# Optimization experiments

Hardware: AMD Instinct MI355X
Metric: run time of the kernel (lower is better)

The kernel has to match this reference:

```python
import jax, jax.numpy as jnp
import numpy as np

B, S, D, H = 4, 1024, 1024, 16
DH = D // H  # 64, per-head dim; FFN hidden = 2048
DFF = 2048

def setup_inputs() -> dict:
    key = jax.random.key(0)
    ks = jax.random.split(key, 6)
    x = jax.random.normal(ks[0], (B, S, D), dtype=jnp.float32)
    # Per-head q/k/v projection weights, stacked over heads: [H, D, DH].
    # Equivalent math to n_heads separate SelfAttentionLayer(d_head) calls + concat.
    sc_in = 1.0 / np.sqrt(D)
    Wq = jax.random.normal(ks[1], (H, D, DH), dtype=jnp.float32) * sc_in
    Wk = jax.random.normal(ks[2], (H, D, DH), dtype=jnp.float32) * sc_in
    Wv = jax.random.normal(ks[3], (H, D, DH), dtype=jnp.float32) * sc_in
    W1 = jax.random.normal(ks[4], (D, DFF), dtype=jnp.float32) * sc_in
    b1 = jnp.zeros((DFF,), dtype=jnp.float32)
    W2 = jax.random.normal(ks[5], (DFF, D), dtype=jnp.float32) * (1.0 / np.sqrt(DFF))
    b2 = jnp.zeros((D,), dtype=jnp.float32)
    return {"x": x, "Wq": Wq, "Wk": Wk, "Wv": Wv,
            "W1": W1, "b1": b1, "W2": W2, "b2": b2}

def reference(x, Wq, Wk, Wv, W1, b1, W2, b2):
    # Batched multi-head self-attention (math-equivalent to the per-head loop + concat).
    q = jnp.einsum('bsd,hde->bhse', x, Wq)          # [B,H,S,DH]
    k = jnp.einsum('bsd,hde->bhse', x, Wk)
    v = jnp.einsum('bsd,hde->bhse', x, Wv)
    scale = 1.0 / jnp.sqrt(jnp.asarray(q.shape[-1], q.dtype))
    scores = jnp.einsum('bhqe,bhke->bhqk', q, k) * scale  # [B,H,S,S]
    attn = jax.nn.softmax(scores, axis=-1)
    o = jnp.einsum('bhqk,bhke->bhqe', attn, v)      # [B,H,S,DH]
    h1 = o.transpose(0, 2, 1, 3).reshape(x.shape[0], x.shape[1], -1)  # concat heads -> [B,S,D]
    # FCLayer(2048, d): Dense(2048, relu) -> Dense(d)
    y = jax.nn.relu(h1 @ W1 + b1) @ W2 + b2
    return y
```

## Files before the change

### kernel.cpp

```cpp
#include <hip/hip_runtime.h>
#include <hip/hip_bf16.h>


typedef unsigned short u16;
typedef __attribute__((ext_vector_type(8))) short bfrag8;
typedef __attribute__((ext_vector_type(4))) float f32x4;
typedef __attribute__((ext_vector_type(4))) int ix4;

constexpr int Bb = 4, Ss = 1024, Dd = 1024, Hh = 16, DFF = 2048;
constexpr float QSCALE = 0.18033688011112042f;

__device__ __forceinline__ u16 f2bf(float f) {
  unsigned u = __float_as_uint(f);
  return (u16)((u + 0x7fffu + ((u >> 16) & 1u)) >> 16);
}

__device__ __forceinline__ void gload16(const void* g, void* l) {
  __builtin_amdgcn_global_load_lds(
      (const __attribute__((address_space(1))) unsigned int*)g,
      (__attribute__((address_space(3))) unsigned int*)l, 16, 0, 0);
}

__device__ __forceinline__ int xcd_swz() {
  const int id = blockIdx.y * gridDim.x + blockIdx.x;
  const int cpx = (gridDim.x * gridDim.y) >> 3;
  return (id & 7) * cpx + (id >> 3);
}

__global__ __launch_bounds__(256) void cvt_bf16(const float* __restrict__ in,
                                                u16* __restrict__ out, int n4) {
  int i = blockIdx.x * 256 + threadIdx.x;
  if (i >= n4) return;
  float4 v = ((const float4*)in)[i];
  ushort4 o = make_ushort4(f2bf(v.x), f2bf(v.y), f2bf(v.z), f2bf(v.w));
  *(ushort4*)(out + (size_t)i * 4) = o;
}

__device__ __forceinline__ void transpose64(const float* __restrict__ in,
                                            u16* __restrict__ out,
                                            int R, int C, int r0, int c0) {
  __shared__ float tile[64][65];
  const int t = threadIdx.x, cl = t & 63, rq = t >> 6;
#pragma unroll
  for (int i = 0; i < 16; ++i) {
    int rl = rq * 16 + i;
    tile[rl][cl] = in[(size_t)(r0 + rl) * C + c0 + cl];
  }
  __syncthreads();
#pragma unroll
  for (int i = 0; i < 16; ++i) {
    int oc = rq * 16 + i;
    out[(size_t)(c0 + oc) * R + r0 + cl] = f2bf(tile[cl][oc]);
  }
}

__global__ __launch_bounds__(256) void transpose_cvt(const float* __restrict__ in,
                                                     u16* __restrict__ out,
                                                     int R, int C) {
  transpose64(in, out, R, C, blockIdx.x * 64, blockIdx.y * 64);
}

__global__ __launch_bounds__(256) void qkv_transpose_cvt(
    const float* __restrict__ Wq, const float* __restrict__ Wk,
    const float* __restrict__ Wv, u16* __restrict__ out) {
  const int z = blockIdx.y;
  const int which = z >> 4, h = z & 15;
  const float* in = (which == 0 ? Wq : which == 1 ? Wk : Wv) + (size_t)h * 1024 * 64;
  u16* o = out + (size_t)z * 64 * 1024;
  transpose64(in, o, 1024, 64, blockIdx.x * 64, 0);
}

template <int EPI>
__global__ __launch_bounds__(256) void mfma_gemm(
    const u16* __restrict__ A, const u16* __restrict__ Bt,
    const float* __restrict__ bias, void* __restrict__ Cout, int N, int K) {
  __shared__ alignas(16) u16 Asm[128 * 32];
  __shared__ alignas(16) u16 Bsm[128 * 32];
  const int tid = threadIdx.x;
  const int wid = tid >> 6, lane = tid & 63;
  const int nid = xcd_swz();
  const int m0 = (nid / gridDim.x) * 128, n0 = (nid % gridDim.x) * 128;
  const int wr = wid >> 1, wc = wid & 1;
  const int fr = lane & 15, krow = lane >> 4;

  const int srow = tid >> 2;
  const int sk = (tid & 3) * 8;
  const u16* ga0 = A + (size_t)(m0 + srow) * K + sk;
  const u16* ga1 = A + (size_t)(m0 + srow + 64) * K + sk;
  const u16* gb0 = Bt + (size_t)(n0 + srow) * K + sk;
  const u16* gb1 = Bt + (size_t)(n0 + srow + 64) * K + sk;
  char* lA0 = (char*)Asm + tid * 16;
  char* lA1 = lA0 + 4096;
  char* lB0 = (char*)Bsm + tid * 16;
  char* lB1 = lB0 + 4096;

  f32x4 acc[4][4];
#pragma unroll
  for (int i = 0; i < 4; ++i)
#pragma unroll
    for (int j = 0; j < 4; ++j) acc[i][j] = (f32x4){0.f, 0.f, 0.f, 0.f};

  const char* pa = (const char*)Asm + (wr * 64 + fr) * 64 + krow * 16;
  const char* pb = (const char*)Bsm + (wc * 64 + fr) * 64 + krow * 16;

  for (int kt = 0; kt < K / 32; ++kt) {
    __syncthreads();
    gload16(ga0 + kt * 32, lA0);
    gload16(ga1 + kt * 32, lA1);
    gload16(gb0 + kt * 32, lB0);
    gload16(gb1 + kt * 32, lB1);
    __syncthreads();

    bfrag8 af[4], bfv[4];
#pragma unroll
    for (int i = 0; i < 4; ++i) af[i] = *(const bfrag8*)(pa + i * 1024);
#pragma unroll
    for (int j = 0; j < 4; ++j) bfv[j] = *(const bfrag8*)(pb + j * 1024);
#pragma unroll
    for (int i = 0; i < 4; ++i)
#pragma unroll
      for (int j = 0; j < 4; ++j)
        acc[i][j] = __builtin_amdgcn_mfma_f32_16x16x32_bf16(af[i], bfv[j], acc[i][j], 0, 0, 0);
  }

  const int orow = (lane >> 4) * 4;
  const int ocol = lane & 15;
#pragma unroll
  for (int i = 0; i < 4; ++i) {
#pragma unroll
    for (int j = 0; j < 4; ++j) {
      const int gn = n0 + wc * 64 + j * 16 + ocol;
      const int gm0 = m0 + wr * 64 + i * 16 + orow;
      if (EPI == 0) {
        const int which = gn >> 10, hh = (gn >> 6) & 15, e = gn & 63;
        const int bb = gm0 >> 10, s0 = gm0 & 1023;
        const int hb = hh * 4 + bb;
        u16* oq = (u16*)Cout;
        if (which == 0) {
#pragma unroll
          for (int r = 0; r < 4; ++r)
            oq[((size_t)hb * 1024 + s0 + r) * 64 + e] = f2bf(acc[i][j][r] * QSCALE);
        } else if (which == 1) {
#pragma unroll
          for (int r = 0; r < 4; ++r)
            oq[4194304 + ((size_t)hb * 1024 + s0 + r) * 64 + e] = f2bf(acc[i][j][r]);
        } else {
          ushort4 pk = make_ushort4(f2bf(acc[i][j][0]), f2bf(acc[i][j][1]),
                                    f2bf(acc[i][j][2]), f2bf(acc[i][j][3]));
          *(ushort4*)&oq[8388608 + ((size_t)hb * 64 + e) * 1024 + s0] = pk;
        }
      } else if (EPI == 1) {
#pragma unroll
        for (int r = 0; r < 4; ++r) {
          float v = fmaxf(acc[i][j][r] + bias[gn], 0.f);
          ((u16*)Cout)[(size_t)(gm0 + r) * N + gn] = f2bf(v);
        }
      } else {
#pragma unroll
        for (int r = 0; r < 4; ++r)
          ((float*)Cout)[(size_t)(gm0 + r) * N + gn] = acc[i][j][r] + bias[gn];
      }
    }
  }
}

__global__ __launch_bounds__(256) void mfma_gemm_n64(
    const u16* __restrict__ A, const u16* __restrict__ Bt,
    const float* __restrict__ bias, float* __restrict__ Cout, int N, int K) {
  __shared__ alignas(16) u16 Asm[128 * 32];
  __shared__ alignas(16) u16 Bsm[64 * 32];
  const int tid = threadIdx.x;
  const int wid = tid >> 6, lane = tid & 63;
  const int nid = xcd_swz();
  const int m0 = (nid / gridDim.x) * 128, n0 = (nid % gridDim.x) * 64;
  const int fr = lane & 15, krow = lane >> 4;

  const int srow = tid >> 2;
  const int sk = (tid & 3) * 8;
  const u16* ga0 = A + (size_t)(m0 + srow) * K + sk;
  const u16* ga1 = A + (size_t)(m0 + srow + 64) * K + sk;
  const u16* gb0 = Bt + (size_t)(n0 + srow) * K + sk;
  char* lA0 = (char*)Asm + tid * 16;
  char* lA1 = lA0 + 4096;
  char* lB0 = (char*)Bsm + tid * 16;

  f32x4 acc[2][4];
#pragma unroll
  for (int i = 0; i < 2; ++i)
#pragma unroll
    for (int j = 0; j < 4; ++j) acc[i][j] = (f32x4){0.f, 0.f, 0.f, 0.f};

  const char* pa = (const char*)Asm + (wid * 32 + fr) * 64 + krow * 16;
  const char* pb = (const char*)Bsm + fr * 64 + krow * 16;

  for (int kt = 0; kt < K / 32; ++kt) {
    __syncthreads();
    gload16(ga0 + kt * 32, lA0);
    gload16(ga1 + kt * 32, lA1);
    gload16(gb0 + kt * 32, lB0);
    __syncthreads();

    bfrag8 af[2], bfv[4];
#pragma unroll
    for (int i = 0; i < 2; ++i) af[i] = *(const bfrag8*)(pa + i * 1024);
#pragma unroll
    for (int j = 0; j < 4; ++j) bfv[j] = *(const bfrag8*)(pb + j * 1024);
#pragma unroll
    for (int i = 0; i < 2; ++i)
#pragma unroll
      for (int j = 0; j < 4; ++j)
        acc[i][j] = __builtin_amdgcn_mfma_f32_16x16x32_bf16(af[i], bfv[j], acc[i][j], 0, 0, 0);
  }

  const int orow = (lane >> 4) * 4;
  const int ocol = lane & 15;
#pragma unroll
  for (int i = 0; i < 2; ++i)
#pragma unroll
    for (int j = 0; j < 4; ++j) {
      const int gn = n0 + j * 16 + ocol;
      const int gm0 = m0 + wid * 32 + i * 16 + orow;
#pragma unroll
      for (int r = 0; r < 4; ++r)
        Cout[(size_t)(gm0 + r) * N + gn] = acc[i][j][r] + bias[gn];
    }
}

__global__ __launch_bounds__(256, 2) void attn_mfma(
    const u16* __restrict__ qb, const u16* __restrict__ kb,
    const u16* __restrict__ vtb, u16* __restrict__ h1) {
  const int tid = threadIdx.x, wid = tid >> 6, lane = tid & 63;
  const int nid = xcd_swz();
  const int qx = nid & 7, hb = nid >> 3;
  const int h = hb >> 2, b = hb & 3;
  const int q0 = qx * 128 + wid * 32;
  const int fr = lane & 15, hi = lane >> 4;

  const u16* Qg = qb + ((size_t)hb * 1024 + q0) * 64;
  const u16* Kg = kb + (size_t)hb * 1024 * 64;
  const u16* Vg = vtb + (size_t)hb * 64 * 1024;

  bfrag8 qf[2][2];
#pragma unroll
  for (int m = 0; m < 2; ++m)
#pragma unroll
    for (int kk = 0; kk < 2; ++kk)
      qf[m][kk] = *(const bfrag8*)(Qg + (m * 16 + fr) * 64 + kk * 32 + hi * 8);

  f32x4 acc2[2][4];
#pragma unroll
  for (int m = 0; m < 2; ++m)
#pragma unroll
    for (int en = 0; en < 4; ++en) acc2[m][en] = (f32x4){0.f, 0.f, 0.f, 0.f};
  float mrun[2] = {-1e30f, -1e30f}, lrun[2] = {0.f, 0.f};

  const int addrA = ((lane & 15) + ((lane & 16) << 1)) << 2;
  const int addrB = addrA + 64;
  const bool hiSel = (lane >= 32);

  bfrag8 kfA[4][2], vfA[4][2], kfB[4][2], vfB[4][2];

#define LOAD_KV(kf, vf, kt)                                                    \
  {                                                                            \
    _Pragma("unroll") for (int kn = 0; kn < 4; ++kn)                           \
        _Pragma("unroll") for (int kk = 0; kk < 2; ++kk) {                     \
      kf[kn][kk] = *(const bfrag8*)(Kg + (size_t)((kt)*64 + kn * 16 + fr) * 64 \
                                    + kk * 32 + hi * 8);                       \
      vf[kn][kk] = *(const bfrag8*)(Vg + (size_t)(kn * 16 + fr) * 1024         \
                                    + (kt)*64 + kk * 32 + hi * 8);             \
    }                                                                          \
  }

#define TILE_STEP(kf, vf)                                                      \
  {                                                                            \
    f32x4 sc2[2][4];                                                           \
    __builtin_amdgcn_s_setprio(1);                                             \
    _Pragma("unroll") for (int m = 0; m < 2; ++m)                              \
        _Pragma("unroll") for (int kn = 0; kn < 4; ++kn) {                     \
      f32x4 t = (f32x4){0.f, 0.f, 0.f, 0.f};                                   \
      t = __builtin_amdgcn_mfma_f32_16x16x32_bf16(kf[kn][0], qf[m][0], t, 0, 0, 0); \
      t = __builtin_amdgcn_mfma_f32_16x16x32_bf16(kf[kn][1], qf[m][1], t, 0, 0, 0); \
      sc2[m][kn] = t;                                                          \
    }                                                                          \
    __builtin_amdgcn_s_setprio(0);                                             \
    int pk[2][4][2];                                                           \
    _Pragma("unroll") for (int m = 0; m < 2; ++m) {                            \
      float cm = -1e30f;                                                       \
      _Pragma("unroll") for (int kn = 0; kn < 4; ++kn)                         \
          _Pragma("unroll") for (int r = 0; r < 4; ++r)                        \
              cm = fmaxf(cm, sc2[m][kn][r]);                                   \
      cm = fmaxf(cm, __shfl_xor(cm, 16));                                      \
      cm = fmaxf(cm, __shfl_xor(cm, 32));                                      \
      const float mnew = fmaxf(mrun[m], cm);                                   \
      const float scl = exp2f(mrun[m] - mnew);                                 \
      mrun[m] = mnew;                                                          \
      float psum = 0.f;                                                        \
      float p[4][4];                                                           \
      _Pragma("unroll") for (int kn = 0; kn < 4; ++kn)                         \
          _Pragma("unroll") for (int r = 0; r < 4; ++r) {                      \
        p[kn][r] = exp2f(sc2[m][kn][r] - mnew);                                \
        psum += p[kn][r];                                                      \
      }                                                                        \
      psum += __shfl_xor(psum, 16);                                            \
      psum += __shfl_xor(psum, 32);                                            \
      lrun[m] = lrun[m] * scl + psum;                                          \
      _Pragma("unroll") for (int en = 0; en < 4; ++en)                         \
          acc2[m][en] = acc2[m][en] * scl;                                     \
      _Pragma("unroll") for (int kn = 0; kn < 4; ++kn) {                       \
        asm("v_cvt_pk_bf16_f32 %0, %1, %2"                                     \
            : "=v"(pk[m][kn][0]) : "v"(p[kn][0]), "v"(p[kn][1]));              \
        asm("v_cvt_pk_bf16_f32 %0, %1, %2"                                     \
            : "=v"(pk[m][kn][1]) : "v"(p[kn][2]), "v"(p[kn][3]));              \
      }                                                                        \
    }                                                                          \
    bfrag8 pfrag[2][2];                                                        \
    _Pragma("unroll") for (int m = 0; m < 2; ++m)                              \
        _Pragma("unroll") for (int kk = 0; kk < 2; ++kk) {                     \
      int w[4];                                                                \
      _Pragma("unroll") for (int wi = 0; wi < 2; ++wi) {                       \
        int t0 = __builtin_amdgcn_ds_bpermute(addrA, pk[m][2 * kk][wi]);       \
        int t1 = __builtin_amdgcn_ds_bpermute(addrA, pk[m][2 * kk + 1][wi]);   \
        w[wi] = hiSel ? t1 : t0;                                               \
        t0 = __builtin_amdgcn_ds_bpermute(addrB, pk[m][2 * kk][wi]);           \
        t1 = __builtin_amdgcn_ds_bpermute(addrB, pk[m][2 * kk + 1][wi]);       \
        w[2 + wi] = hiSel ? t1 : t0;                                           \
      }                                                                        \
      ix4 tmp = (ix4){w[0], w[1], w[2], w[3]};                                 \
      pfrag[m][kk] = __builtin_bit_cast(bfrag8, tmp);                          \
    }                                                                          \
    __builtin_amdgcn_s_setprio(1);                                             \
    _Pragma("unroll") for (int m = 0; m < 2; ++m)                              \
        _Pragma("unroll") for (int en = 0; en < 4; ++en) {                     \
      acc2[m][en] = __builtin_amdgcn_mfma_f32_16x16x32_bf16(                   \
          vf[en][0], pfrag[m][0], acc2[m][en], 0, 0, 0);                       \
      acc2[m][en] = __builtin_amdgcn_mfma_f32_16x16x32_bf16(                   \
          vf[en][1], pfrag[m][1], acc2[m][en], 0, 0, 0);                       \
    }                                                                          \
    __builtin_amdgcn_s_setprio(0);                                             \
  }

  LOAD_KV(kfA, vfA, 0);
  for (int kt = 0; kt < 16; kt += 2) {
    if (kt + 1 < 16) LOAD_KV(kfB, vfB, kt + 1);
    TILE_STEP(kfA, vfA);
    if (kt + 2 < 16) LOAD_KV(kfA, vfA, kt + 2);
    TILE_STEP(kfB, vfB);
  }

#pragma unroll
  for (int m = 0; m < 2; ++m) {
    const float inv = 1.f / lrun[m];
    const int s = q0 + m * 16 + fr;
    u16* op = h1 + ((size_t)(b * 1024 + s)) * 1024 + h * 64 + hi * 4;
#pragma unroll
    for (int en = 0; en < 4; ++en) {
      ushort4 o = make_ushort4(
          f2bf(acc2[m][en][0] * inv), f2bf(acc2[m][en][1] * inv),
          f2bf(acc2[m][en][2] * inv), f2bf(acc2[m][en][3] * inv));
      *(ushort4*)(op + en * 16) = o;
    }
  }
#undef LOAD_KV
#undef TILE_STEP
}

extern "C" void kernel_launch(void* const* d_in, const int* in_sizes, int n_in,
                              void* d_out, int out_size, void* d_ws, size_t ws_size,
                              hipStream_t stream) {
  const float* x  = (const float*)d_in[0];
  const float* Wq = (const float*)d_in[1];
  const float* Wk = (const float*)d_in[2];
  const float* Wv = (const float*)d_in[3];
  const float* W1 = (const float*)d_in[4];
  const float* b1 = (const float*)d_in[5];
  const float* W2 = (const float*)d_in[6];
  const float* b2 = (const float*)d_in[7];

  const size_t MB = 1u << 20;
  char* w = (char*)d_ws;
  u16* qkvb  = (u16*)w;
  u16* Xb    = (u16*)(w + 24 * MB);
  u16* Wqkvt = (u16*)(w + 32 * MB);
  u16* W1t   = (u16*)(w + 38 * MB);
  u16* W2t   = (u16*)(w + 42 * MB);
  u16* h1b   = (u16*)(w + 46 * MB);
  u16* ffb   = (u16*)(w + 54 * MB);

  cvt_bf16<<<4096, 256, 0, stream>>>(x, Xb, 1048576);
  qkv_transpose_cvt<<<dim3(16, 48), 256, 0, stream>>>(Wq, Wk, Wv, Wqkvt);
  transpose_cvt<<<dim3(16, 32), 256, 0, stream>>>(W1, W1t, 1024, 2048);
  transpose_cvt<<<dim3(32, 16), 256, 0, stream>>>(W2, W2t, 2048, 1024);

  mfma_gemm<0><<<dim3(24, 32), 256, 0, stream>>>(Xb, Wqkvt, nullptr, qkvb, 3072, 1024);
  attn_mfma<<<dim3(8, 64), 256, 0, stream>>>(qkvb, qkvb + 4194304, qkvb + 8388608, h1b);
  mfma_gemm<1><<<dim3(16, 32), 256, 0, stream>>>(h1b, W1t, b1, ffb, 2048, 1024);
  mfma_gemm_n64<<<dim3(16, 32), 256, 0, stream>>>(ffb, W2t, b2, (float*)d_out, 1024, 2048);
}
```

Measured before the change: 279.1 us.

## Rewrite attention with 32x32x16 MFMA tiles and permlane32 swap for P repack

Switches the attention kernel from 16x16x32 MFMA fragments to 32x32x16 MFMA, so each wave handles 32 query rows as a single tile. The softmax cross-lane reductions drop to one shuffle, and the ds_bpermute-based repacking of P into B-operand fragments is replaced with v_permlane32_swap. This reduces LDS-permute traffic and instruction count in the softmax stage. In exchange it drops the explicit double-buffered K/V register prefetch, so load latency relies on the compiler and on occupancy to hide it.

```diff
diff --git a/kernel.cpp b/kernel.cpp
--- a/kernel.cpp
+++ b/kernel.cpp
@@ -5,6 +5,7 @@
 typedef unsigned short u16;
 typedef __attribute__((ext_vector_type(8))) short bfrag8;
 typedef __attribute__((ext_vector_type(4))) float f32x4;
+typedef __attribute__((ext_vector_type(16))) float f32x16;
 typedef __attribute__((ext_vector_type(4))) int ix4;
 
 constexpr int Bb = 4, Ss = 1024, Dd = 1024, Hh = 16, DFF = 2048;
@@ -226,142 +227,124 @@
     }
 }
 
-__global__ __launch_bounds__(256, 2) void attn_mfma(
+__global__ __launch_bounds__(256, 2) void attn_mfma32(
     const u16* __restrict__ qb, const u16* __restrict__ kb,
     const u16* __restrict__ vtb, u16* __restrict__ h1) {
-  const int tid = threadIdx.x, wid = tid >> 6, lane = tid & 63;
+  const int wid = threadIdx.x >> 6, lane = threadIdx.x & 63;
   const int nid = xcd_swz();
   const int qx = nid & 7, hb = nid >> 3;
   const int h = hb >> 2, b = hb & 3;
   const int q0 = qx * 128 + wid * 32;
-  const int fr = lane & 15, hi = lane >> 4;
-
-  const u16* Qg = qb + ((size_t)hb * 1024 + q0) * 64;
-  const u16* Kg = kb + (size_t)hb * 1024 * 64;
-  const u16* Vg = vtb + (size_t)hb * 64 * 1024;
-
-  bfrag8 qf[2][2];
-#pragma unroll
-  for (int m = 0; m < 2; ++m)
-#pragma unroll
-    for (int kk = 0; kk < 2; ++kk)
-      qf[m][kk] = *(const bfrag8*)(Qg + (m * 16 + fr) * 64 + kk * 32 + hi * 8);
-
-  f32x4 acc2[2][4];
-#pragma unroll
-  for (int m = 0; m < 2; ++m)
-#pragma unroll
-    for (int en = 0; en < 4; ++en) acc2[m][en] = (f32x4){0.f, 0.f, 0.f, 0.f};
-  float mrun[2] = {-1e30f, -1e30f}, lrun[2] = {0.f, 0.f};
-
-  const int addrA = ((lane & 15) + ((lane & 16) << 1)) << 2;
-  const int addrB = addrA + 64;
-  const bool hiSel = (lane >= 32);
-
-  bfrag8 kfA[4][2], vfA[4][2], kfB[4][2], vfB[4][2];
-
-#define LOAD_KV(kf, vf, kt)                                                    \
+  const int ql = lane & 31, hi = lane >> 5;
+
+  const u16* Qp  = qb + ((size_t)hb * 1024 + q0 + ql) * 64 + hi * 8;
+  const u16* Kp0 = kb + (size_t)hb * 65536 + (size_t)ql * 64 + hi * 8;
+  const u16* Kp1 = Kp0 + 32 * 64;
+  const u16* Vp0 = vtb + (size_t)hb * 65536 + (size_t)ql * 1024 + hi * 8;
+  const u16* Vp1 = Vp0 + 32 * 1024;
+
+  bfrag8 qf[4];
+#pragma unroll
+  for (int st = 0; st < 4; ++st) qf[st] = *(const bfrag8*)(Qp + st * 16);
+
+  f32x16 po0, po1;
+#pragma unroll
+  for (int i = 0; i < 16; ++i) { po0[i] = 0.f; po1[i] = 0.f; }
+  float mrun = -1e30f, lrun = 0.f;
+
+#define PACK4(dst, p, base)                                                    \
   {                                                                            \
-    _Pragma("unroll") for (int kn = 0; kn < 4; ++kn)                           \
-        _Pragma("unroll") for (int kk = 0; kk < 2; ++kk) {                     \
-      kf[kn][kk] = *(const bfrag8*)(Kg + (size_t)((kt)*64 + kn * 16 + fr) * 64 \
-                                    + kk * 32 + hi * 8);                       \
-      vf[kn][kk] = *(const bfrag8*)(Vg + (size_t)(kn * 16 + fr) * 1024         \
-                                    + (kt)*64 + kk * 32 + hi * 8);             \
-    }                                                                          \
-  }
-
-#define TILE_STEP(kf, vf)                                                      \
-  {                                                                            \
-    f32x4 sc2[2][4];                                                           \
-    __builtin_amdgcn_s_setprio(1);                                             \
-    _Pragma("unroll") for (int m = 0; m < 2; ++m)                              \
-        _Pragma("unroll") for (int kn = 0; kn < 4; ++kn) {                     \
-      f32x4 t = (f32x4){0.f, 0.f, 0.f, 0.f};                                   \
-      t = __builtin_amdgcn_mfma_f32_16x16x32_bf16(kf[kn][0], qf[m][0], t, 0, 0, 0); \
-      t = __builtin_amdgcn_mfma_f32_16x16x32_bf16(kf[kn][1], qf[m][1], t, 0, 0, 0); \
-      sc2[m][kn] = t;                                                          \
-    }                                                                          \
-    __builtin_amdgcn_s_setprio(0);                                             \
-    int pk[2][4][2];                                                           \
-    _Pragma("unroll") for (int m = 0; m < 2; ++m) {                            \
-      float cm = -1e30f;                                                       \
-      _Pragma("unroll") for (int kn = 0; kn < 4; ++kn)                         \
-          _Pragma("unroll") for (int r = 0; r < 4; ++r)                        \
-              cm = fmaxf(cm, sc2[m][kn][r]);                                   \
-      cm = fmaxf(cm, __shfl_xor(cm, 16));                                      \
-      cm = fmaxf(cm, __shfl_xor(cm, 32));                                      \
-      const float mnew = fmaxf(mrun[m], cm);                                   \
-      const float scl = exp2f(mrun[m] - mnew);                                 \
-      mrun[m] = mnew;                                                          \
-      float psum = 0.f;                                                        \
-      float p[4][4];                                                           \
-      _Pragma("unroll") for (int kn = 0; kn < 4; ++kn)                         \
-          _Pragma("unroll") for (int r = 0; r < 4; ++r) {                      \
-        p[kn][r] = exp2f(sc2[m][kn][r] - mnew);                                \
-        psum += p[kn][r];                                                      \
-      }                                                                        \
-      psum += __shfl_xor(psum, 16);                                            \
-      psum += __shfl_xor(psum, 32);                                            \
-      lrun[m] = lrun[m] * scl + psum;                                          \
-      _Pragma("unroll") for (int en = 0; en < 4; ++en)                         \
-          acc2[m][en] = acc2[m][en] * scl;                                     \
-      _Pragma("unroll") for (int kn = 0; kn < 4; ++kn) {                       \
-        asm("v_cvt_pk_bf16_f32 %0, %1, %2"                                     \
-            : "=v"(pk[m][kn][0]) : "v"(p[kn][0]), "v"(p[kn][1]));              \
-        asm("v_cvt_pk_bf16_f32 %0, %1, %2"                                     \
-            : "=v"(pk[m][kn][1]) : "v"(p[kn][2]), "v"(p[kn][3]));              \
-      }                                                                        \
-    }                                                                          \
-    bfrag8 pfrag[2][2];                                                        \
-    _Pragma("unroll") for (int m = 0; m < 2; ++m)                              \
-        _Pragma("unroll") for (int kk = 0; kk < 2; ++kk) {                     \
-      int w[4];                                                                \
-      _Pragma("unroll") for (int wi = 0; wi < 2; ++wi) {                       \
-        int t0 = __builtin_amdgcn_ds_bpermute(addrA, pk[m][2 * kk][wi]);       \
-        int t1 = __builtin_amdgcn_ds_bpermute(addrA, pk[m][2 * kk + 1][wi]);   \
-        w[wi] = hiSel ? t1 : t0;                                               \
-        t0 = __builtin_amdgcn_ds_bpermute(addrB, pk[m][2 * kk][wi]);           \
-        t1 = __builtin_amdgcn_ds_bpermute(addrB, pk[m][2 * kk + 1][wi]);       \
-        w[2 + wi] = hiSel ? t1 : t0;                                           \
-      }                                                                        \
-      ix4 tmp = (ix4){w[0], w[1], w[2], w[3]};                                 \
-      pfrag[m][kk] = __builtin_bit_cast(bfrag8, tmp);                          \
-    }                                                                          \
-    __builtin_amdgcn_s_setprio(1);                                             \
-    _Pragma("unroll") for (int m = 0; m < 2; ++m)                              \
-        _Pragma("unroll") for (int en = 0; en < 4; ++en) {                     \
-      acc2[m][en] = __builtin_amdgcn_mfma_f32_16x16x32_bf16(                   \
-          vf[en][0], pfrag[m][0], acc2[m][en], 0, 0, 0);                       \
-      acc2[m][en] = __builtin_amdgcn_mfma_f32_16x16x32_bf16(                   \
-          vf[en][1], pfrag[m][1], acc2[m][en], 0, 0, 0);                       \
-    }                                                                          \
-    __builtin_amdgcn_s_setprio(0);                                             \
-  }
-
-  LOAD_KV(kfA, vfA, 0);
-  for (int kt = 0; kt < 16; kt += 2) {
-    if (kt + 1 < 16) LOAD_KV(kfB, vfB, kt + 1);
-    TILE_STEP(kfA, vfA);
-    if (kt + 2 < 16) LOAD_KV(kfA, vfA, kt + 2);
-    TILE_STEP(kfB, vfB);
-  }
-
-#pragma unroll
-  for (int m = 0; m < 2; ++m) {
-    const float inv = 1.f / lrun[m];
-    const int s = q0 + m * 16 + fr;
-    u16* op = h1 + ((size_t)(b * 1024 + s)) * 1024 + h * 64 + hi * 4;
-#pragma unroll
-    for (int en = 0; en < 4; ++en) {
-      ushort4 o = make_ushort4(
-          f2bf(acc2[m][en][0] * inv), f2bf(acc2[m][en][1] * inv),
-          f2bf(acc2[m][en][2] * inv), f2bf(acc2[m][en][3] * inv));
-      *(ushort4*)(op + en * 16) = o;
-    }
-  }
-#undef LOAD_KV
-#undef TILE_STEP
+    int a0, a1, b0, b1;                                                        \
+    asm("v_cvt_pk_bf16_f32 %0, %1, %2" : "=v"(a0)                              \
+        : "v"(p[base + 0]), "v"(p[base + 1]));                                 \
+    asm("v_cvt_pk_bf16_f32 %0, %1, %2" : "=v"(a1)                              \
+        : "v"(p[base + 2]), "v"(p[base + 3]));                                 \
+    asm("v_cvt_pk_bf16_f32 %0, %1, %2" : "=v"(b0)                              \
+        : "v"(p[base + 4]), "v"(p[base + 5]));                                 \
+    asm("v_cvt_pk_bf16_f32 %0, %1, %2" : "=v"(b1)                              \
+        : "v"(p[base + 6]), "v"(p[base + 7]));                                 \
+    asm("v_permlane32_swap_b32 %0, %1" : "+v"(a0), "+v"(b0));                  \
+    asm("v_permlane32_swap_b32 %0, %1" : "+v"(a1), "+v"(b1));                  \
+    ix4 t = (ix4){a0, a1, b0, b1};                                             \
+    dst = __builtin_bit_cast(bfrag8, t);                                       \
+  }
+
+  for (int kt = 0; kt < 16; ++kt) {
+    const u16* k0 = Kp0 + kt * 4096;
+    const u16* k1 = Kp1 + kt * 4096;
+    const u16* v0 = Vp0 + kt * 64;
+    const u16* v1 = Vp1 + kt * 64;
+    bfrag8 kf0[4], kf1[4], vf0[4], vf1[4];
+#pragma unroll
+    for (int st = 0; st < 4; ++st) {
+      kf0[st] = *(const bfrag8*)(k0 + st * 16);
+      kf1[st] = *(const bfrag8*)(k1 + st * 16);
+      vf0[st] = *(const bfrag8*)(v0 + st * 16);
+      vf1[st] = *(const bfrag8*)(v1 + st * 16);
+    }
+
+    f32x16 pa0, pa1;
+#pragma unroll
+    for (int i = 0; i < 16; ++i) { pa0[i] = 0.f; pa1[i] = 0.f; }
+    __builtin_amdgcn_s_setprio(1);
+#pragma unroll
+    for (int st = 0; st < 4; ++st) {
+      pa0 = __builtin_amdgcn_mfma_f32_32x32x16_bf16(kf0[st], qf[st], pa0, 0, 0, 0);
+      pa1 = __builtin_amdgcn_mfma_f32_32x32x16_bf16(kf1[st], qf[st], pa1, 0, 0, 0);
+    }
+    __builtin_amdgcn_s_setprio(0);
+
+    float cm = fmaxf(pa0[0], pa1[0]);
+#pragma unroll
+    for (int i = 1; i < 16; ++i) cm = fmaxf(cm, fmaxf(pa0[i], pa1[i]));
+    cm = fmaxf(cm, __shfl_xor(cm, 32));
+    const float mnew = fmaxf(mrun, cm);
+    const float scl = exp2f(mrun - mnew);
+    mrun = mnew;
+    float psum = 0.f;
+#pragma unroll
+    for (int i = 0; i < 16; ++i) {
+      pa0[i] = exp2f(pa0[i] - mnew);
+      pa1[i] = exp2f(pa1[i] - mnew);
+      psum += pa0[i] + pa1[i];
+    }
+    psum += __shfl_xor(psum, 32);
+    lrun = lrun * scl + psum;
+    po0 *= scl;
+    po1 *= scl;
+
+    bfrag8 pf00, pf01, pf10, pf11;
+    PACK4(pf00, pa0, 0);
+    PACK4(pf01, pa0, 8);
+    PACK4(pf10, pa1, 0);
+    PACK4(pf11, pa1, 8);
+
+    __builtin_amdgcn_s_setprio(1);
+    po0 = __builtin_amdgcn_mfma_f32_32x32x16_bf16(vf0[0], pf00, po0, 0, 0, 0);
+    po0 = __builtin_amdgcn_mfma_f32_32x32x16_bf16(vf0[1], pf01, po0, 0, 0, 0);
+    po0 = __builtin_amdgcn_mfma_f32_32x32x16_bf16(vf0[2], pf10, po0, 0, 0, 0);
+    po0 = __builtin_amdgcn_mfma_f32_32x32x16_bf16(vf0[3], pf11, po0, 0, 0, 0);
+    po1 = __builtin_amdgcn_mfma_f32_32x32x16_bf16(vf1[0], pf00, po1, 0, 0, 0);
+    po1 = __builtin_amdgcn_mfma_f32_32x32x16_bf16(vf1[1], pf01, po1, 0, 0, 0);
+    po1 = __builtin_amdgcn_mfma_f32_32x32x16_bf16(vf1[2], pf10, po1, 0, 0, 0);
+    po1 = __builtin_amdgcn_mfma_f32_32x32x16_bf16(vf1[3], pf11, po1, 0, 0, 0);
+    __builtin_amdgcn_s_setprio(0);
+  }
+#undef PACK4
+
+  const float inv = 1.f / lrun;
+  u16* orow = h1 + ((size_t)(b * 1024 + q0 + ql)) * 1024 + h * 64 + hi * 4;
+#pragma unroll
+  for (int r4 = 0; r4 < 4; ++r4) {
+    ushort4 o0 = make_ushort4(
+        f2bf(po0[r4 * 4 + 0] * inv), f2bf(po0[r4 * 4 + 1] * inv),
+        f2bf(po0[r4 * 4 + 2] * inv), f2bf(po0[r4 * 4 + 3] * inv));
+    *(ushort4*)(orow + r4 * 8) = o0;
+    ushort4 o1 = make_ushort4(
+        f2bf(po1[r4 * 4 + 0] * inv), f2bf(po1[r4 * 4 + 1] * inv),
+        f2bf(po1[r4 * 4 + 2] * inv), f2bf(po1[r4 * 4 + 3] * inv));
+    *(ushort4*)(orow + 32 + r4 * 8) = o1;
+  }
 }
 
 extern "C" void kernel_launch(void* const* d_in, const int* in_sizes, int n_in,
@@ -392,7 +375,7 @@
   transpose_cvt<<<dim3(32, 16), 256, 0, stream>>>(W2, W2t, 2048, 1024);
 
   mfma_gemm<0><<<dim3(24, 32), 256, 0, stream>>>(Xb, Wqkvt, nullptr, qkvb, 3072, 1024);
-  attn_mfma<<<dim3(8, 64), 256, 0, stream>>>(qkvb, qkvb + 4194304, qkvb + 8388608, h1b);
+  attn_mfma32<<<dim3(8, 64), 256, 0, stream>>>(qkvb, qkvb + 4194304, qkvb + 8388608, h1b);
   mfma_gemm<1><<<dim3(16, 32), 256, 0, stream>>>(h1b, W1t, b1, ffb, 2048, 1024);
   mfma_gemm_n64<<<dim3(16, 32), 256, 0, stream>>>(ffb, W2t, b2, (float*)d_out, 1024, 2048);
 }
```

New measurement: 275.1 us. Within noise of the previous version (-1.4%).
